# Kernel tuning notes

Hardware: AMD Instinct MI355X
Metric: run time of the kernel (lower is better)

## Reference

```python
import jax, jax.numpy as jnp
import numpy as np


def setup_inputs() -> dict:
    key = jax.random.key(0)
    k1, k2 = jax.random.split(key)
    B, T, C = 32, 512, 384
    MAX_LEN = 4096
    x = jax.random.normal(k1, (B, T, C), dtype=jnp.float32)
    duration = jax.random.randint(k2, (B, T), 0, 12, dtype=jnp.int64)
    return {"x": x, "duration": duration, "max_len": MAX_LEN}


def reference(x, duration, max_len):
    # x: [B, T, C] float; duration: [B, T] int; max_len: python int
    B, T, C = x.shape
    dur = jnp.maximum(duration, 0)            # original clamps expand_size at 0
    csum = jnp.cumsum(dur, axis=1)            # [B, T] exclusive boundaries (right edges)
    pos = jnp.arange(max_len)                 # [max_len]
    # source phoneme index for each output frame j: count of csum[b] <= j
    idx = jax.vmap(lambda c: jnp.searchsorted(c, pos, side="right"))(csum)  # [B, max_len]
    idx_c = jnp.clip(idx, 0, T - 1)
    out = jnp.take_along_axis(x, idx_c[:, :, None], axis=1)  # [B, max_len, C]
    mel_len = csum[:, -1]                     # [B] total expanded frames per batch
    valid = pos[None, :] < mel_len[:, None]   # [B, max_len], pad region -> 0
    out = out * valid[:, :, None].astype(out.dtype)
    return out, mel_len
```

## Files before the change

kernel.cpp:

```cpp
#include <hip/hip_runtime.h>
#include <hip/hip_bf16.h>


#define B  32
#define T  512
#define C  384
#define C4 96
#define ML 4096
#define PPB 128

__global__ void lr_scan_kernel(const int* __restrict__ dur,
                               int* __restrict__ csum,
                               float* __restrict__ mel_out) {
    __shared__ int s[T];
    const int b = blockIdx.x;
    const int t = threadIdx.x;

    int v = dur[b * T + t];
    if (v < 0) v = 0;
    s[t] = v;
    __syncthreads();

    for (int off = 1; off < T; off <<= 1) {
        int add = (t >= off) ? s[t - off] : 0;
        __syncthreads();
        s[t] += add;
        __syncthreads();
    }

    csum[b * T + t] = s[t];
    if (t == T - 1) mel_out[b] = (float)s[T - 1];
}

__global__ __launch_bounds__(256)
void lr_expand_kernel(const float* __restrict__ x,
                      const int* __restrict__ csum,
                      float* __restrict__ out) {
    __shared__ int s_cs[T];
    __shared__ int s_idx[PPB];

    const int tilesPerBatch = ML / PPB;
    const int b     = blockIdx.x / tilesPerBatch;
    const int ptile = blockIdx.x % tilesPerBatch;
    const int tid   = threadIdx.x;

    for (int i = tid; i < T; i += 256) s_cs[i] = csum[b * T + i];
    __syncthreads();

    const int mel = s_cs[T - 1];

    if (tid < PPB) {
        const int p = ptile * PPB + tid;
        int r = -1;
        if (p < mel) {
            int lo = 0, hi = T;
            while (lo < hi) {
                int mid = (lo + hi) >> 1;
                if (s_cs[mid] <= p) lo = mid + 1; else hi = mid;
            }
            r = lo < (T - 1) ? lo : (T - 1);
        }
        s_idx[tid] = r;
    }
    __syncthreads();

    const float4* __restrict__ x4 = (const float4*)x;
    float4* __restrict__ o4 = (float4*)out;
    const size_t xrow_base = (size_t)b * T * C4;
    const size_t obase = (size_t)b * ML * C4 + (size_t)ptile * PPB * C4;

    const float4 zero = make_float4(0.f, 0.f, 0.f, 0.f);
    #pragma unroll 4
    for (int v = tid; v < PPB * C4; v += 256) {
        const int pl = v / C4;
        const int c4 = v - pl * C4;
        const int t  = s_idx[pl];
        float4 val = zero;
        if (t >= 0) val = x4[xrow_base + (size_t)t * C4 + c4];
        o4[obase + v] = val;
    }
}

extern "C" void kernel_launch(void* const* d_in, const int* in_sizes, int n_in,
                              void* d_out, int out_size, void* d_ws, size_t ws_size,
                              hipStream_t stream) {
    const float* x   = (const float*)d_in[0];
    const int*   dur = (const int*)d_in[1];

    float* out     = (float*)d_out;
    float* mel_out = out + (size_t)B * ML * C;
    int*   csum    = (int*)d_ws;

    lr_scan_kernel<<<B, T, 0, stream>>>(dur, csum, mel_out);

    const int grid = B * (ML / PPB);
    lr_expand_kernel<<<grid, 256, 0, stream>>>(x, csum, out);
}
```

Measured before the change: 232.8 us.

## Fuse duration scan into expand kernel and use nontemporal output stores

Removes the separate prefix-sum kernel and its workspace round trip. Each expand block now recomputes the cumulative durations for its batch row in shared memory, with every thread scanning a pair of elements. Output writes switch to nontemporal stores so the large streamed output does not pollute the cache. The cost is redundant per-block scan work (32 tiles per batch) and one fewer kernel launch and dependency.

```diff
diff --git a/kernel.cpp b/kernel.cpp
--- a/kernel.cpp
+++ b/kernel.cpp
@@ -2,41 +2,23 @@
 #include <hip/hip_bf16.h>
 
 
-#define B  32
-#define T  512
-#define C  384
-#define C4 96
-#define ML 4096
+#define B   32
+#define T   512
+#define C   384
+#define C4  96
+#define ML  4096
 #define PPB 128
+#define TPB 256
 
-__global__ void lr_scan_kernel(const int* __restrict__ dur,
-                               int* __restrict__ csum,
-                               float* __restrict__ mel_out) {
-    __shared__ int s[T];
-    const int b = blockIdx.x;
-    const int t = threadIdx.x;
+typedef float v4f __attribute__((ext_vector_type(4)));
 
-    int v = dur[b * T + t];
-    if (v < 0) v = 0;
-    s[t] = v;
-    __syncthreads();
-
-    for (int off = 1; off < T; off <<= 1) {
-        int add = (t >= off) ? s[t - off] : 0;
-        __syncthreads();
-        s[t] += add;
-        __syncthreads();
-    }
-
-    csum[b * T + t] = s[t];
-    if (t == T - 1) mel_out[b] = (float)s[T - 1];
-}
-
-__global__ __launch_bounds__(256)
-void lr_expand_kernel(const float* __restrict__ x,
-                      const int* __restrict__ csum,
-                      float* __restrict__ out) {
+__global__ __launch_bounds__(TPB)
+void lr_fused_kernel(const float* __restrict__ x,
+                     const int* __restrict__ dur,
+                     float* __restrict__ out,
+                     float* __restrict__ mel_out) {
     __shared__ int s_cs[T];
+    __shared__ int s_p[TPB];
     __shared__ int s_idx[PPB];
 
     const int tilesPerBatch = ML / PPB;
@@ -44,10 +26,25 @@
     const int ptile = blockIdx.x % tilesPerBatch;
     const int tid   = threadIdx.x;
 
-    for (int i = tid; i < T; i += 256) s_cs[i] = csum[b * T + i];
+    int2 d2 = ((const int2*)(dur + b * T))[tid];
+    int d0 = d2.x < 0 ? 0 : d2.x;
+    int d1 = d2.y < 0 ? 0 : d2.y;
+    s_p[tid] = d0 + d1;
+    __syncthreads();
+    #pragma unroll
+    for (int off = 1; off < TPB; off <<= 1) {
+        int add = (tid >= off) ? s_p[tid - off] : 0;
+        __syncthreads();
+        s_p[tid] += add;
+        __syncthreads();
+    }
+    const int S = s_p[tid];
+    s_cs[2 * tid + 1] = S;
+    s_cs[2 * tid]     = S - d1;
     __syncthreads();
 
     const int mel = s_cs[T - 1];
+    if (ptile == 0 && tid == 0) mel_out[b] = (float)mel;
 
     if (tid < PPB) {
         const int p = ptile * PPB + tid;
@@ -64,20 +61,20 @@
     }
     __syncthreads();
 
-    const float4* __restrict__ x4 = (const float4*)x;
-    float4* __restrict__ o4 = (float4*)out;
-    const size_t xrow_base = (size_t)b * T * C4;
+    const v4f* __restrict__ x4 = (const v4f*)x;
+    v4f* __restrict__ o4 = (v4f*)out;
+    const size_t xbase = (size_t)b * T * C4;
     const size_t obase = (size_t)b * ML * C4 + (size_t)ptile * PPB * C4;
+    const v4f zero = (v4f){0.f, 0.f, 0.f, 0.f};
 
-    const float4 zero = make_float4(0.f, 0.f, 0.f, 0.f);
     #pragma unroll 4
-    for (int v = tid; v < PPB * C4; v += 256) {
+    for (int v = tid; v < PPB * C4; v += TPB) {
         const int pl = v / C4;
         const int c4 = v - pl * C4;
         const int t  = s_idx[pl];
-        float4 val = zero;
-        if (t >= 0) val = x4[xrow_base + (size_t)t * C4 + c4];
-        o4[obase + v] = val;
+        v4f val = zero;
+        if (t >= 0) val = x4[xbase + (size_t)t * C4 + c4];
+        __builtin_nontemporal_store(val, &o4[obase + v]);
     }
 }
 
@@ -89,10 +86,7 @@
 
     float* out     = (float*)d_out;
     float* mel_out = out + (size_t)B * ML * C;
-    int*   csum    = (int*)d_ws;
-
-    lr_scan_kernel<<<B, T, 0, stream>>>(dur, csum, mel_out);
 
     const int grid = B * (ML / PPB);
-    lr_expand_kernel<<<grid, 256, 0, stream>>>(x, csum, out);
+    lr_fused_kernel<<<grid, TPB, 0, stream>>>(x, dur, out, mel_out);
 }
```

New measurement: 239.3 us. 2.8% more time.
